# Optimization experiments

Hardware: AMD Instinct MI355X
Metric: run time of the kernel (lower is better)

Reference implementation:

```python
import jax, jax.numpy as jnp
import numpy as np

B, N = 2, 2048
N_FEAT, N_HID, N_HEADS, N_CLASS = 256, 64, 8, 16
ALPHA = 0.2  # leakyrelu negative slope
NEG_INF = -1.0e12


def _xavier_uniform(key, shape, gain=1.414):
    fan_in, fan_out = shape[-2], shape[-1]
    bound = gain * np.sqrt(6.0 / (fan_in + fan_out))
    return jax.random.uniform(key, shape, jnp.float32, -bound, bound)


def setup_inputs() -> dict:
    key = jax.random.key(0)
    k_x, k_adj, k_w, k_a, k_wo, k_ao = jax.random.split(key, 6)
    x = jax.random.normal(k_x, (B, N, N_FEAT), jnp.float32)
    adj = (jax.random.uniform(k_adj, (B, N, N)) < 0.005).astype(jnp.float32)
    adj = jnp.maximum(adj, jnp.eye(N, dtype=jnp.float32))  # self loops
    Ws = _xavier_uniform(k_w, (N_HEADS, N_FEAT, N_HID))
    As = _xavier_uniform(k_a, (N_HEADS, 2 * N_HID, 1))
    W_out = _xavier_uniform(k_wo, (N_HID * N_HEADS, N_CLASS))
    a_out = _xavier_uniform(k_ao, (2 * N_CLASS, 1))
    return {"x": x, "adj": adj, "Ws": Ws, "As": As,
            "W_out": W_out, "a_out": a_out, "d_window": 3}


def init_weight_graph(adj, d_window):
    # Faithful vectorized version of GAT.init_weight_graph (the per-batch
    # python loop is just a vmap over batch; adj_graphs list is dead code).
    Nn = adj.shape[-1]
    eye = jnp.eye(Nn, dtype=adj.dtype)
    sigma2 = 2.0 * (d_window / 2.0) ** 2
    # NOTE: original uses np.exp(-1 ** 2 / sigma2) == exp(-1/sigma2) (python precedence)
    weight = eye + np.float32(np.exp(-1.0 / sigma2)) * (adj - eye)
    prev = adj
    for i in range(d_window - 1):
        e_prev = jnp.einsum('bij,bkj->bik', prev, adj)          # prev @ adj^T
        e_ret = (e_prev > 0).astype(adj.dtype)
        e_graph = ((e_ret - prev) > 0).astype(adj.dtype)
        weight = weight + np.float32(np.exp(-(i + 2) ** 2 / sigma2)) * e_graph
        prev = e_ret
    return weight  # [B, N, N]


def gat_layer(x, W, a, adjw, concat):
    h = jnp.einsum('bnf,fo->bno', x, W)                         # [B,N,F_out]
    F_out = W.shape[1]
    # cat([h_i, h_j]) @ a  ==  (h@a1)_i + (h@a2)_j  (exact same math, no N^2*2F tensor)
    f1 = jnp.einsum('bno,o->bn', h, a[:F_out, 0])
    f2 = jnp.einsum('bno,o->bn', h, a[F_out:, 0])
    e = jax.nn.leaky_relu(f1[:, :, None] + f2[:, None, :], ALPHA)  # [B,N,N]
    attention = jnp.where(adjw > 0, adjw * e, NEG_INF)
    attention = jax.nn.softmax(attention, axis=2)
    # dropout is a no-op in eval mode
    h_prime = jnp.einsum('bnm,bmo->bno', attention, h)
    return jax.nn.elu(h_prime) if concat else h_prime


def reference(x, adj, Ws, As, W_out, a_out, d_window):
    adjw = init_weight_graph(adj, d_window)
    # multi-head layers (concat=True), vmapped over heads then concatenated
    heads = jax.vmap(lambda W, a: gat_layer(x, W, a, adjw, True))(Ws, As)  # [H,B,N,nhid]
    Hh, Bb, Nn, Fh = heads.shape
    xh = jnp.moveaxis(heads, 0, 2).reshape(Bb, Nn, Hh * Fh)
    out = gat_layer(xh, W_out, a_out, adjw, False)
    return jax.nn.elu(out)  # [B, N, n_class]
```

## Files before the change

kernel.cpp:

```cpp
#include <hip/hip_runtime.h>
#include <stdint.h>

#define NB 2
#define NN 2048
#define NF 256
#define NHID 64
#define NH 8
#define NC 16
#define NW 64
#define LRA 0.2f

constexpr double L2E_D = 1.4426950408889634;
constexpr float L2E  = (float)L2E_D;
constexpr float K12  = (float)((0.8007374029168081 - 0.4111122905071874) * L2E_D);
constexpr float K23  = (float)((0.4111122905071874 - 0.1353352832366127) * L2E_D);
constexpr float K3L  = (float)(0.1353352832366127 * L2E_D);
constexpr float KD   = K12 + (K23 + K3L);
constexpr float GB   = 1e30f;

using short8  = __attribute__((ext_vector_type(8))) short;
using floatx4 = __attribute__((ext_vector_type(4))) float;
union Frag { short8 v; uint32_t w[4]; };

__device__ __forceinline__ float bf2f(uint16_t h){ return __uint_as_float(((uint32_t)h) << 16); }
__device__ __forceinline__ uint16_t f2bf(float f){
  uint32_t u = __float_as_uint(f);
  return (uint16_t)((u + 0x7FFFu + ((u >> 16) & 1u)) >> 16);
}
__device__ __forceinline__ float lrelu(float x){ return fmaxf(x, LRA * x); }
__device__ __forceinline__ void pack2(float p0, float p1, uint32_t& hi, uint32_t& lo){
  uint32_t u0 = __float_as_uint(p0), u1 = __float_as_uint(p1);
  hi = __builtin_amdgcn_perm(u1, u0, 0x07060302u);
  float t0 = p0 - __uint_as_float(u0 & 0xFFFF0000u);
  float t1 = p1 - __uint_as_float(u1 & 0xFFFF0000u);
  lo = __builtin_amdgcn_perm(__float_as_uint(t1), __float_as_uint(t0), 0x07060302u);
}
__device__ __forceinline__ uint32_t packrn2(float p0, float p1){
  uint32_t u0 = __float_as_uint(p0), u1 = __float_as_uint(p1);
  u0 += 0x7FFFu + ((u0 >> 16) & 1u);
  u1 += 0x7FFFu + ((u1 >> 16) & 1u);
  return __builtin_amdgcn_perm(u1, u0, 0x07060302u);
}

__global__ void __launch_bounds__(256) k_pack(const uint32_t* __restrict__ adj,
                                              const float* __restrict__ Ws,
                                              uint32_t* __restrict__ adjR,
                                              uint32_t* __restrict__ colB,
                                              uint16_t* __restrict__ WTh,
                                              uint16_t* __restrict__ WTl){
  __shared__ uint32_t tile[64][65];
  int jc = blockIdx.x, kc = blockIdx.y, b = blockIdx.z;
  int t = threadIdx.x, lane = t & 63, w = t >> 6;
  int k0 = kc * 64, j0 = jc * 64;
  const uint32_t* base = adj + ((size_t)b * NN + k0) * NN + j0;
  for (int s = 0; s < 16; ++s){
    int r = w * 16 + s;
    tile[r][lane] = base[(size_t)r * NN + lane] << 1;
  }
  __syncthreads();
  for (int s = 0; s < 16; ++s){
    int r = s * 4 + w;
    uint64_t mr = __ballot(tile[r][lane] != 0u);
    if (lane < 2) adjR[((size_t)b * NN + k0 + r) * NW + jc * 2 + lane] = (uint32_t)(mr >> (32 * lane));
    uint64_t mc = __ballot(tile[lane][r] != 0u);
    if (lane < 2) colB[((size_t)b * NN + j0 + r) * NW + kc * 2 + lane] = (uint32_t)(mc >> (32 * lane));
  }
  if (kc == 0 && b == 0 && jc < NH){
    int hd = jc;
    const float* src = Ws + (size_t)hd * NF * NHID;
    for (int s = 0; s < 64; ++s){
      int f = s * 4 + (t >> 6), o = t & 63;
      float v = src[(size_t)f * NHID + o];
      uint16_t hi = f2bf(v);
      uint16_t lo = f2bf(v - bf2f(hi));
      WTh[(size_t)hd * NHID * NF + (size_t)o * NF + f] = hi;
      WTl[(size_t)hd * NHID * NF + (size_t)o * NF + f] = lo;
    }
  }
}

__global__ void __launch_bounds__(256, 4) k_rh(const uint32_t* __restrict__ adjR,
                                               const uint32_t* __restrict__ colB,
                                               uint32_t* __restrict__ cmb,
                                               const float* __restrict__ x,
                                               const uint16_t* __restrict__ WTh,
                                               const uint16_t* __restrict__ WTl,
                                               const float* __restrict__ As,
                                               uint16_t* __restrict__ hTh,
                                               float* __restrict__ f1,
                                               float* __restrict__ f2){
  __shared__ float hbuf[16][65];
  int t = threadIdx.x, lane = t & 63, w = t >> 6;
  if (blockIdx.x < 1024){
    int row = blockIdx.x * 4 + w;
    int b = row >> 11;
    const uint32_t* colb = colB + (size_t)b * NN * NW + lane;
    uint32_t myadj = adjR[(size_t)row * NW + lane];
    uint32_t acc2 = 0;
    for (int ww = 0; ww < 64; ++ww){
      uint32_t bits = __shfl(myadj, ww);
      const uint32_t* cb = colb + (size_t)(ww * 32) * NW;
      while (bits){
        int b0 = __ffs(bits) - 1;              bits &= bits - 1;
        int b1 = bits ? __ffs(bits) - 1 : b0;  bits &= bits - 1;
        int b2 = bits ? __ffs(bits) - 1 : b0;  bits &= bits - 1;
        int b3 = bits ? __ffs(bits) - 1 : b0;  bits &= bits - 1;
        uint32_t v0 = cb[(size_t)b0 * NW];
        uint32_t v1 = cb[(size_t)b1 * NW];
        uint32_t v2 = cb[(size_t)b2 * NW];
        uint32_t v3 = cb[(size_t)b3 * NW];
        acc2 |= (v0 | v1) | (v2 | v3);
      }
    }
    uint32_t acc3 = 0;
    for (int ww = 0; ww < 64; ++ww){
      uint32_t bits = __shfl(acc2, ww);
      const uint32_t* cb = colb + (size_t)(ww * 32) * NW;
      while (bits){
        int b0 = __ffs(bits) - 1;              bits &= bits - 1;
        int b1 = bits ? __ffs(bits) - 1 : b0;  bits &= bits - 1;
        int b2 = bits ? __ffs(bits) - 1 : b0;  bits &= bits - 1;
        int b3 = bits ? __ffs(bits) - 1 : b0;  bits &= bits - 1;
        uint32_t v0 = cb[(size_t)b0 * NW];
        uint32_t v1 = cb[(size_t)b1 * NW];
        uint32_t v2 = cb[(size_t)b2 * NW];
        uint32_t v3 = cb[(size_t)b3 * NW];
        acc3 |= (v0 | v1) | (v2 | v3);
      }
    }
    uint32_t* cw = cmb + ((size_t)row * NW + lane) * 3;
    cw[0] = myadj; cw[1] = acc2; cw[2] = acc3;
  } else {
    int bid2 = blockIdx.x - 1024;
    int itile = bid2 & 127, hd = (bid2 >> 7) & 7, b = bid2 >> 10;
    int q = lane >> 4, m = lane & 15;
    int n0 = itile * 16;
    floatx4 acc = {0.f, 0.f, 0.f, 0.f};
    const float*    xrow = x   + ((size_t)b * NN + n0 + m) * NF;
    const uint16_t* wth  = WTh + ((size_t)hd * NHID + w * 16 + m) * NF;
    const uint16_t* wtl  = WTl + ((size_t)hd * NHID + w * 16 + m) * NF;
    for (int k0 = 0; k0 < NF; k0 += 32){
      float4 xa = *(const float4*)(xrow + k0 + q * 8);
      float4 xb = *(const float4*)(xrow + k0 + q * 8 + 4);
      float xv[8] = {xa.x, xa.y, xa.z, xa.w, xb.x, xb.y, xb.z, xb.w};
      Frag ah, al;
      #pragma unroll
      for (int k = 0; k < 4; ++k) pack2(xv[2*k], xv[2*k+1], ah.w[k], al.w[k]);
      short8 bh = *(const short8*)(wth + k0 + q * 8);
      short8 bl = *(const short8*)(wtl + k0 + q * 8);
      acc = __builtin_amdgcn_mfma_f32_16x16x32_bf16(ah.v, bh, acc, 0, 0, 0);
      acc = __builtin_amdgcn_mfma_f32_16x16x32_bf16(al.v, bh, acc, 0, 0, 0);
      acc = __builtin_amdgcn_mfma_f32_16x16x32_bf16(ah.v, bl, acc, 0, 0, 0);
    }
    #pragma unroll
    for (int v = 0; v < 4; ++v) hbuf[q * 4 + v][w * 16 + m] = acc[v];
    __syncthreads();
    {
      int o = t >> 2, nb = (t & 3) * 4;
      uint64_t pkh = 0;
      for (int s = 0; s < 4; ++s)
        pkh |= (uint64_t)f2bf(hbuf[nb + s][o]) << (16 * s);
      size_t off = ((size_t)(b * NH + hd) * NHID + o) * NN + n0 + nb;
      *(uint64_t*)(hTh + off) = pkh;
    }
    float a1v = As[hd * 128 + lane];
    float a2v = As[hd * 128 + 64 + lane];
    for (int s = 0; s < 4; ++s){
      int row = w * 4 + s;
      float hv = hbuf[row][lane];
      float v1 = hv * a1v, v2 = hv * a2v;
      for (int d = 1; d < 64; d <<= 1){ v1 += __shfl_xor(v1, d); v2 += __shfl_xor(v2, d); }
      if (lane == 0){
        f1[(size_t)(b * NH + hd) * NN + n0 + row] = v1;
        f2[(size_t)(b * NH + hd) * NN + n0 + row] = v2;
      }
    }
  }
}

__global__ void __launch_bounds__(512) k_attn1(const uint32_t* __restrict__ cmb,
                                               const float* __restrict__ f1,
                                               const float* __restrict__ f2,
                                               const uint16_t* __restrict__ hTh,
                                               float* __restrict__ xh){
  int combo = blockIdx.x * 2 + blockIdx.y;
  int hd = combo & 7, b = combo >> 3;
  int itile = blockIdx.z;
  int t = threadIdx.x, lane = t & 63, w = t >> 6;
  int q = lane >> 4, m = lane & 15;
  int i0 = itile * 32;
  int igA = i0 + m, igB = i0 + 16 + m;
  const float* f1p = f1 + (size_t)(b * NH + hd) * NN;
  const float* f2p = f2 + (size_t)(b * NH + hd) * NN;
  float f1A = f1p[igA], f1B = f1p[igB];
  const uint32_t* cA = cmb + ((size_t)b * NN + igA) * (NW * 3);
  const uint32_t* cB = cmb + ((size_t)b * NN + igB) * (NW * 3);
  size_t hoff = (size_t)(b * NH + hd) * NHID * NN;
  const uint16_t* hhp = hTh + hoff;
  int jlo = w * 256, sh = q * 8;
  floatx4 aA0 = {0.f,0.f,0.f,0.f}, aA1 = aA0, aA2 = aA0, aA3 = aA0;
  floatx4 aB0 = aA0, aB1 = aA0, aB2 = aA0, aB3 = aA0;
  float lsA = 0.f, lsB = 0.f;
  for (int s = 0; s < 8; ++s){
    int j0 = jlo + s * 32;
    int wi = j0 >> 5;
    const uint32_t* cwA = cA + wi * 3;
    const uint32_t* cwB = cB + wi * 3;
    uint32_t waA = cwA[0] >> sh, w2A = cwA[1] >> sh, w3A = cwA[2] >> sh;
    uint32_t waB = cwB[0] >> sh, w2B = cwB[1] >> sh, w3B = cwB[2] >> sh;
    const float4 fa = *(const float4*)(f2p + j0 + sh);
    const float4 fb = *(const float4*)(f2p + j0 + sh + 4);
    float f2v[8] = {fa.x, fa.y, fa.z, fa.w, fb.x, fb.y, fb.z, fb.w};
    float pvA[8], pvB[8];
    #pragma unroll
    for (int u = 0; u < 8; ++u){
      float eA = lrelu(f1A + f2v[u]);
      float b1 = (float)((waA >> u) & 1u);
      float b2 = (float)((w2A >> u) & 1u);
      float b3 = (float)((w3A >> u) & 1u);
      float Ks = fmaf(b1, K12, fmaf(b2, K23, K3L));
      float p = exp2f(fmaf(eA, Ks, fmaf(b3, GB, -GB)));
      pvA[u] = p; lsA += p;
      float eB = lrelu(f1B + f2v[u]);
      float c1 = (float)((waB >> u) & 1u);
      float c2 = (float)((w2B >> u) & 1u);
      float c3 = (float)((w3B >> u) & 1u);
      float Kt = fmaf(c1, K12, fmaf(c2, K23, K3L));
      float pb = exp2f(fmaf(eB, Kt, fmaf(c3, GB, -GB)));
      pvB[u] = pb; lsB += pb;
    }
    Frag ahA, ahB;
    #pragma unroll
    for (int k = 0; k < 4; ++k){
      ahA.w[k] = packrn2(pvA[2*k], pvA[2*k+1]);
      ahB.w[k] = packrn2(pvB[2*k], pvB[2*k+1]);
    }
    const uint16_t* hrow_h = hhp + j0 + sh;
    #pragma unroll
    for (int blk = 0; blk < 4; ++blk){
      size_t ro = (size_t)(blk * 16 + m) * NN;
      short8 bh = *(const short8*)(hrow_h + ro);
      floatx4* apA = (blk == 0) ? &aA0 : (blk == 1) ? &aA1 : (blk == 2) ? &aA2 : &aA3;
      floatx4* apB = (blk == 0) ? &aB0 : (blk == 1) ? &aB1 : (blk == 2) ? &aB2 : &aB3;
      *apA = __builtin_amdgcn_mfma_f32_16x16x32_bf16(ahA.v, bh, *apA, 0, 0, 0);
      *apB = __builtin_amdgcn_mfma_f32_16x16x32_bf16(ahB.v, bh, *apB, 0, 0, 0);
    }
  }
  lsA += __shfl_xor(lsA, 16); lsA += __shfl_xor(lsA, 32);
  lsB += __shfl_xor(lsB, 16); lsB += __shfl_xor(lsB, 32);
  __shared__ float redO[4][32][66];
  __shared__ float redl[8][32];
  if (lane < 16) redl[w][lane] = lsA;
  else if (lane < 32) redl[w][16 + (lane & 15)] = lsB;
  if (w < 4){
    #pragma unroll
    for (int v = 0; v < 4; ++v){
      int r = q * 4 + v;
      redO[w][r][ 0 + m] = aA0[v];
      redO[w][r][16 + m] = aA1[v];
      redO[w][r][32 + m] = aA2[v];
      redO[w][r][48 + m] = aA3[v];
      redO[w][16 + r][ 0 + m] = aB0[v];
      redO[w][16 + r][16 + m] = aB1[v];
      redO[w][16 + r][32 + m] = aB2[v];
      redO[w][16 + r][48 + m] = aB3[v];
    }
  }
  __syncthreads();
  if (w >= 4){
    int wb = w - 4;
    #pragma unroll
    for (int v = 0; v < 4; ++v){
      int r = q * 4 + v;
      redO[wb][r][ 0 + m] += aA0[v];
      redO[wb][r][16 + m] += aA1[v];
      redO[wb][r][32 + m] += aA2[v];
      redO[wb][r][48 + m] += aA3[v];
      redO[wb][16 + r][ 0 + m] += aB0[v];
      redO[wb][16 + r][16 + m] += aB1[v];
      redO[wb][16 + r][32 + m] += aB2[v];
      redO[wb][16 + r][48 + m] += aB3[v];
    }
  }
  __syncthreads();
  int col = t & 63, r0 = t >> 6;
  const float* f1row = f1p + i0;
  #pragma unroll
  for (int s2 = 0; s2 < 4; ++s2){
    int row = s2 * 8 + r0;
    int i = i0 + row;
    float ov = (redO[0][row][col] + redO[1][row][col]) + (redO[2][row][col] + redO[3][row][col]);
    float lv = ((redl[0][row] + redl[1][row]) + (redl[2][row] + redl[3][row]))
             + ((redl[4][row] + redl[5][row]) + (redl[6][row] + redl[7][row]));
    float eii = lrelu(f1row[row] + f2p[i]);
    float pcorr = exp2f(eii * L2E) - exp2f(eii * KD);
    float hic = bf2f(hhp[(size_t)col * NN + i]);
    ov += pcorr * hic;
    lv += pcorr;
    lv = fmaxf(lv, 1e-30f);
    float vv = ov / lv;
    vv = vv > 0.f ? vv : expm1f(vv);
    xh[(size_t)(b * NN + i) * (NH * NHID) + hd * NHID + col] = vv;
  }
}

__global__ void __launch_bounds__(256) k_outprep(const float* __restrict__ xh,
                                                 const float* __restrict__ W_out,
                                                 const float* __restrict__ a_out,
                                                 uint16_t* __restrict__ h2Th,
                                                 float* __restrict__ f12,
                                                 float* __restrict__ f22){
  int t = threadIdx.x, lane = t & 63, w = t >> 6;
  int row = blockIdx.x * 4 + w;
  int b = row >> 11, n = row & (NN - 1);
  int o = lane & 15, c = lane >> 4;
  const float* xr = xh + (size_t)row * (NH * NHID) + c * 128;
  const float* wp = W_out + (size_t)(c * 128) * NC + o;
  float a0 = 0.f, a1 = 0.f, a2 = 0.f, a3 = 0.f;
  #pragma unroll 4
  for (int f = 0; f < 128; f += 4){
    float4 xv = *(const float4*)(xr + f);
    a0 = fmaf(xv.x, wp[(size_t)(f + 0) * NC], a0);
    a1 = fmaf(xv.y, wp[(size_t)(f + 1) * NC], a1);
    a2 = fmaf(xv.z, wp[(size_t)(f + 2) * NC], a2);
    a3 = fmaf(xv.w, wp[(size_t)(f + 3) * NC], a3);
  }
  float acc = (a0 + a1) + (a2 + a3);
  acc += __shfl_xor(acc, 16); acc += __shfl_xor(acc, 32);
  if (lane < 16) h2Th[((size_t)b * NC + o) * NN + n] = f2bf(acc);
  float v1 = acc * a_out[o];
  float v2 = acc * a_out[NC + o];
  for (int d = 1; d < 16; d <<= 1){ v1 += __shfl_xor(v1, d); v2 += __shfl_xor(v2, d); }
  if (lane == 0){ f12[row] = v1; f22[row] = v2; }
}

__global__ void __launch_bounds__(512) k_attn2(const uint32_t* __restrict__ cmb,
                                               const float* __restrict__ f12,
                                               const float* __restrict__ f22,
                                               const uint16_t* __restrict__ h2Th,
                                               float* __restrict__ out){
  int itile = blockIdx.x, b = blockIdx.z;
  int t = threadIdx.x, lane = t & 63, w = t >> 6;
  int q = lane >> 4, m = lane & 15;
  int i0 = itile * 16, ig = i0 + m;
  float f1v = f12[(size_t)b * NN + ig];
  const float*    f2p = f22 + (size_t)b * NN;
  const uint32_t* cA = cmb + ((size_t)b * NN + ig) * (NW * 3);
  const uint16_t* hhp = h2Th + (size_t)b * NC * NN;
  int jlo = w * 256, sh = q * 8;
  floatx4 ac = {0.f,0.f,0.f,0.f};
  float ls0 = 0.f, ls1 = 0.f;
  for (int s = 0; s < 8; ++s){
    int j0 = jlo + s * 32;
    int wi = j0 >> 5;
    const uint32_t* cw = cA + wi * 3;
    uint32_t wa = cw[0] >> sh, w2 = cw[1] >> sh, w3 = cw[2] >> sh;
    const float4 fa = *(const float4*)(f2p + j0 + sh);
    const float4 fb = *(const float4*)(f2p + j0 + sh + 4);
    float f2v[8] = {fa.x, fa.y, fa.z, fa.w, fb.x, fb.y, fb.z, fb.w};
    float pv[8];
    #pragma unroll
    for (int u = 0; u < 8; ++u){
      float e = lrelu(f1v + f2v[u]);
      float b1 = (float)((wa >> u) & 1u);
      float b2 = (float)((w2 >> u) & 1u);
      float b3 = (float)((w3 >> u) & 1u);
      float Ks = fmaf(b1, K12, fmaf(b2, K23, K3L));
      float p = exp2f(fmaf(e, Ks, fmaf(b3, GB, -GB)));
      pv[u] = p;
      if (u & 1) ls1 += p; else ls0 += p;
    }
    Frag afh;
    #pragma unroll
    for (int k = 0; k < 4; ++k) afh.w[k] = packrn2(pv[2*k], pv[2*k+1]);
    size_t ro = (size_t)m * NN + j0 + sh;
    short8 bh = *(const short8*)(hhp + ro);
    ac = __builtin_amdgcn_mfma_f32_16x16x32_bf16(afh.v, bh, ac, 0, 0, 0);
  }
  float lsum = ls0 + ls1;
  lsum += __shfl_xor(lsum, 16); lsum += __shfl_xor(lsum, 32);
  __shared__ float redO[4][16][17];
  __shared__ float redl[8][16];
  if (lane < 16) redl[w][lane] = lsum;
  if (w < 4){
    #pragma unroll
    for (int v = 0; v < 4; ++v) redO[w][q * 4 + v][m] = ac[v];
  }
  __syncthreads();
  if (w >= 4){
    int wb = w - 4;
    #pragma unroll
    for (int v = 0; v < 4; ++v) redO[wb][q * 4 + v][m] += ac[v];
  }
  __syncthreads();
  if (t < 256){
    int col = t & 15, row = t >> 4;
    int i = i0 + row;
    float ov = (redO[0][row][col] + redO[1][row][col]) + (redO[2][row][col] + redO[3][row][col]);
    float lv = ((redl[0][row] + redl[1][row]) + (redl[2][row] + redl[3][row]))
             + ((redl[4][row] + redl[5][row]) + (redl[6][row] + redl[7][row]));
    float eii = lrelu(f12[(size_t)b * NN + i] + f2p[i]);
    float pcorr = exp2f(eii * L2E) - exp2f(eii * KD);
    float hic = bf2f(hhp[(size_t)col * NN + i]);
    ov += pcorr * hic;
    lv += pcorr;
    lv = fmaxf(lv, 1e-30f);
    float vv = ov / lv;
    vv = vv > 0.f ? vv : expm1f(vv);
    out[(size_t)(b * NN + i) * NC + col] = vv;
  }
}

extern "C" void kernel_launch(void* const* d_in, const int* in_sizes, int n_in,
                              void* d_out, int out_size, void* d_ws, size_t ws_size,
                              hipStream_t stream) {
  const float* x        = (const float*)d_in[0];
  const uint32_t* adj_u = (const uint32_t*)d_in[1];
  const float* Ws    = (const float*)d_in[2];
  const float* As    = (const float*)d_in[3];
  const float* W_out = (const float*)d_in[4];
  const float* a_out = (const float*)d_in[5];
  float* out = (float*)d_out;

  char* ws = (char*)d_ws;
  const size_t MB = 1u << 20;
  uint32_t* adjR = (uint32_t*)(ws + 0 * MB);
  uint32_t* colB = (uint32_t*)(ws + 1 * MB);
  uint32_t* cmb  = (uint32_t*)(ws + 2 * MB);
  uint16_t* WTh  = (uint16_t*)(ws + 5 * MB);
  uint16_t* WTl  = (uint16_t*)(ws + 5 * MB + 256 * 1024);
  float*    f1   = (float*)(ws + 5 * MB + 512 * 1024);
  float*    f2   = (float*)(ws + 5 * MB + 640 * 1024);
  uint16_t* hTh  = (uint16_t*)(ws + 6 * MB);
  float*    xh   = (float*)(ws + 14 * MB);
  uint16_t* h2Th = (uint16_t*)(ws + 22 * MB);
  float*    f12  = (float*)(ws + 22 * MB + 256 * 1024);
  float*    f22  = (float*)(ws + 22 * MB + 272 * 1024);

  k_pack   <<<dim3(32, 32, NB), 256, 0, stream>>>(adj_u, Ws, adjR, colB, WTh, WTl);
  k_rh     <<<dim3(1024 + NN / 16 * NH * NB), 256, 0, stream>>>(adjR, colB, cmb,
                                             x, WTh, WTl, As, hTh, f1, f2);
  k_attn1  <<<dim3(8, 2, NN / 32), 512, 0, stream>>>(cmb, f1, f2, hTh, xh);
  k_outprep<<<dim3(1024), 256, 0, stream>>>(xh, W_out, a_out, h2Th, f12, f22);
  k_attn2  <<<dim3(NN / 16, 1, NB), 512, 0, stream>>>(cmb, f12, f22, h2Th, out);
}
```

Measured before the change: 243.4 us.

## Tile attention kernel over two heads per row tile instead of 32 rows

```diff
diff --git a/kernel.cpp b/kernel.cpp
--- a/kernel.cpp
+++ b/kernel.cpp
@@ -183,20 +183,21 @@
                                                const float* __restrict__ f2,
                                                const uint16_t* __restrict__ hTh,
                                                float* __restrict__ xh){
-  int combo = blockIdx.x * 2 + blockIdx.y;
-  int hd = combo & 7, b = combo >> 3;
+  int combo = blockIdx.x;
+  int hp = combo & 3, b = combo >> 2;
+  int h0 = hp * 2, h1 = h0 + 1;
   int itile = blockIdx.z;
   int t = threadIdx.x, lane = t & 63, w = t >> 6;
   int q = lane >> 4, m = lane & 15;
-  int i0 = itile * 32;
-  int igA = i0 + m, igB = i0 + 16 + m;
-  const float* f1p = f1 + (size_t)(b * NH + hd) * NN;
-  const float* f2p = f2 + (size_t)(b * NH + hd) * NN;
-  float f1A = f1p[igA], f1B = f1p[igB];
-  const uint32_t* cA = cmb + ((size_t)b * NN + igA) * (NW * 3);
-  const uint32_t* cB = cmb + ((size_t)b * NN + igB) * (NW * 3);
-  size_t hoff = (size_t)(b * NH + hd) * NHID * NN;
-  const uint16_t* hhp = hTh + hoff;
+  int i0 = itile * 16, ig = i0 + m;
+  const float* f1p0 = f1 + (size_t)(b * NH + h0) * NN;
+  const float* f2p0 = f2 + (size_t)(b * NH + h0) * NN;
+  const float* f1p1 = f1 + (size_t)(b * NH + h1) * NN;
+  const float* f2p1 = f2 + (size_t)(b * NH + h1) * NN;
+  float f1A0 = f1p0[ig], f1A1 = f1p1[ig];
+  const uint32_t* cA = cmb + ((size_t)b * NN + ig) * (NW * 3);
+  const uint16_t* hhp0 = hTh + (size_t)(b * NH + h0) * NHID * NN;
+  const uint16_t* hhp1 = hTh + (size_t)(b * NH + h1) * NHID * NN;
   int jlo = w * 256, sh = q * 8;
   floatx4 aA0 = {0.f,0.f,0.f,0.f}, aA1 = aA0, aA2 = aA0, aA3 = aA0;
   floatx4 aB0 = aA0, aB1 = aA0, aB2 = aA0, aB3 = aA0;
@@ -204,46 +205,46 @@
   for (int s = 0; s < 8; ++s){
     int j0 = jlo + s * 32;
     int wi = j0 >> 5;
-    const uint32_t* cwA = cA + wi * 3;
-    const uint32_t* cwB = cB + wi * 3;
-    uint32_t waA = cwA[0] >> sh, w2A = cwA[1] >> sh, w3A = cwA[2] >> sh;
-    uint32_t waB = cwB[0] >> sh, w2B = cwB[1] >> sh, w3B = cwB[2] >> sh;
-    const float4 fa = *(const float4*)(f2p + j0 + sh);
-    const float4 fb = *(const float4*)(f2p + j0 + sh + 4);
-    float f2v[8] = {fa.x, fa.y, fa.z, fa.w, fb.x, fb.y, fb.z, fb.w};
-    float pvA[8], pvB[8];
+    const uint32_t* cw = cA + wi * 3;
+    uint32_t wa = cw[0] >> sh, w2 = cw[1] >> sh, w3 = cw[2] >> sh;
+    const float4 fa0 = *(const float4*)(f2p0 + j0 + sh);
+    const float4 fb0 = *(const float4*)(f2p0 + j0 + sh + 4);
+    const float4 fa1 = *(const float4*)(f2p1 + j0 + sh);
+    const float4 fb1 = *(const float4*)(f2p1 + j0 + sh + 4);
+    float f2v0[8] = {fa0.x, fa0.y, fa0.z, fa0.w, fb0.x, fb0.y, fb0.z, fb0.w};
+    float f2v1[8] = {fa1.x, fa1.y, fa1.z, fa1.w, fb1.x, fb1.y, fb1.z, fb1.w};
+    float pv0[8], pv1[8];
     #pragma unroll
     for (int u = 0; u < 8; ++u){
-      float eA = lrelu(f1A + f2v[u]);
-      float b1 = (float)((waA >> u) & 1u);
-      float b2 = (float)((w2A >> u) & 1u);
-      float b3 = (float)((w3A >> u) & 1u);
+      float b1 = (float)((wa >> u) & 1u);
+      float b2 = (float)((w2 >> u) & 1u);
+      float b3 = (float)((w3 >> u) & 1u);
       float Ks = fmaf(b1, K12, fmaf(b2, K23, K3L));
-      float p = exp2f(fmaf(eA, Ks, fmaf(b3, GB, -GB)));
-      pvA[u] = p; lsA += p;
-      float eB = lrelu(f1B + f2v[u]);
-      float c1 = (float)((waB >> u) & 1u);
-      float c2 = (float)((w2B >> u) & 1u);
-      float c3 = (float)((w3B >> u) & 1u);
-      float Kt = fmaf(c1, K12, fmaf(c2, K23, K3L));
-      float pb = exp2f(fmaf(eB, Kt, fmaf(c3, GB, -GB)));
-      pvB[u] = pb; lsB += pb;
-    }
-    Frag ahA, ahB;
+      float bias = fmaf(b3, GB, -GB);
+      float e0 = lrelu(f1A0 + f2v0[u]);
+      float p0 = exp2f(fmaf(e0, Ks, bias));
+      pv0[u] = p0; lsA += p0;
+      float e1 = lrelu(f1A1 + f2v1[u]);
+      float p1 = exp2f(fmaf(e1, Ks, bias));
+      pv1[u] = p1; lsB += p1;
+    }
+    Frag ah0, ah1;
     #pragma unroll
     for (int k = 0; k < 4; ++k){
-      ahA.w[k] = packrn2(pvA[2*k], pvA[2*k+1]);
-      ahB.w[k] = packrn2(pvB[2*k], pvB[2*k+1]);
-    }
-    const uint16_t* hrow_h = hhp + j0 + sh;
+      ah0.w[k] = packrn2(pv0[2*k], pv0[2*k+1]);
+      ah1.w[k] = packrn2(pv1[2*k], pv1[2*k+1]);
+    }
+    const uint16_t* hr0 = hhp0 + j0 + sh;
+    const uint16_t* hr1 = hhp1 + j0 + sh;
     #pragma unroll
     for (int blk = 0; blk < 4; ++blk){
       size_t ro = (size_t)(blk * 16 + m) * NN;
-      short8 bh = *(const short8*)(hrow_h + ro);
+      short8 bh0 = *(const short8*)(hr0 + ro);
+      short8 bh1 = *(const short8*)(hr1 + ro);
       floatx4* apA = (blk == 0) ? &aA0 : (blk == 1) ? &aA1 : (blk == 2) ? &aA2 : &aA3;
       floatx4* apB = (blk == 0) ? &aB0 : (blk == 1) ? &aB1 : (blk == 2) ? &aB2 : &aB3;
-      *apA = __builtin_amdgcn_mfma_f32_16x16x32_bf16(ahA.v, bh, *apA, 0, 0, 0);
-      *apB = __builtin_amdgcn_mfma_f32_16x16x32_bf16(ahB.v, bh, *apB, 0, 0, 0);
+      *apA = __builtin_amdgcn_mfma_f32_16x16x32_bf16(ah0.v, bh0, *apA, 0, 0, 0);
+      *apB = __builtin_amdgcn_mfma_f32_16x16x32_bf16(ah1.v, bh1, *apB, 0, 0, 0);
     }
   }
   lsA += __shfl_xor(lsA, 16); lsA += __shfl_xor(lsA, 32);
@@ -284,23 +285,27 @@
   }
   __syncthreads();
   int col = t & 63, r0 = t >> 6;
-  const float* f1row = f1p + i0;
   #pragma unroll
   for (int s2 = 0; s2 < 4; ++s2){
     int row = s2 * 8 + r0;
-    int i = i0 + row;
+    int hsel = row >> 4;
+    int i = i0 + (row & 15);
+    const float* f1e = hsel ? f1p1 : f1p0;
+    const float* f2e = hsel ? f2p1 : f2p0;
+    const uint16_t* hh = hsel ? hhp1 : hhp0;
+    int hdv = hsel ? h1 : h0;
     float ov = (redO[0][row][col] + redO[1][row][col]) + (redO[2][row][col] + redO[3][row][col]);
     float lv = ((redl[0][row] + redl[1][row]) + (redl[2][row] + redl[3][row]))
              + ((redl[4][row] + redl[5][row]) + (redl[6][row] + redl[7][row]));
-    float eii = lrelu(f1row[row] + f2p[i]);
+    float eii = lrelu(f1e[i] + f2e[i]);
     float pcorr = exp2f(eii * L2E) - exp2f(eii * KD);
-    float hic = bf2f(hhp[(size_t)col * NN + i]);
+    float hic = bf2f(hh[(size_t)col * NN + i]);
     ov += pcorr * hic;
     lv += pcorr;
     lv = fmaxf(lv, 1e-30f);
     float vv = ov / lv;
     vv = vv > 0.f ? vv : expm1f(vv);
-    xh[(size_t)(b * NN + i) * (NH * NHID) + hd * NHID + col] = vv;
+    xh[(size_t)(b * NN + i) * (NH * NHID) + hdv * NHID + col] = vv;
   }
 }
 
@@ -440,7 +445,7 @@
   k_pack   <<<dim3(32, 32, NB), 256, 0, stream>>>(adj_u, Ws, adjR, colB, WTh, WTl);
   k_rh     <<<dim3(1024 + NN / 16 * NH * NB), 256, 0, stream>>>(adjR, colB, cmb,
                                              x, WTh, WTl, As, hTh, f1, f2);
-  k_attn1  <<<dim3(8, 2, NN / 32), 512, 0, stream>>>(cmb, f1, f2, hTh, xh);
+  k_attn1  <<<dim3(8, 1, NN / 16), 512, 0, stream>>>(cmb, f1, f2, hTh, xh);
   k_outprep<<<dim3(1024), 256, 0, stream>>>(xh, W_out, a_out, h2Th, f12, f22);
   k_attn2  <<<dim3(NN / 16, 1, NB), 512, 0, stream>>>(cmb, f12, f22, h2Th, out);
 }
```

Result: slower. 265.4 us (+9.0%).

## Compact two-hop neighbor list in LDS and widen attn2 blocks to 16 waves

Applied to the files above, without the earlier changes.

```diff
diff --git a/kernel.cpp b/kernel.cpp
--- a/kernel.cpp
+++ b/kernel.cpp
@@ -9,6 +9,7 @@
 #define NC 16
 #define NW 64
 #define LRA 0.2f
+#define RCAP 1024
 
 constexpr double L2E_D = 1.4426950408889634;
 constexpr float L2E  = (float)L2E_D;
@@ -90,10 +91,11 @@
                                                float* __restrict__ f1,
                                                float* __restrict__ f2){
   __shared__ float hbuf[16][65];
+  __shared__ uint16_t lst[4][RCAP];
   int t = threadIdx.x, lane = t & 63, w = t >> 6;
   if (blockIdx.x < 1024){
     int row = blockIdx.x * 4 + w;
-    int b = row >> 11;
+    int b = row >> 11, iloc = row & (NN - 1);
     const uint32_t* colb = colB + (size_t)b * NN * NW + lane;
     uint32_t myadj = adjR[(size_t)row * NW + lane];
     uint32_t acc2 = 0;
@@ -112,21 +114,43 @@
         acc2 |= (v0 | v1) | (v2 | v3);
       }
     }
+    int cnt = __popc(acc2);
+    int inc = cnt;
+    #pragma unroll
+    for (int d = 1; d < 64; d <<= 1){
+      int v = __shfl_up(inc, d);
+      if (lane >= d) inc += v;
+    }
+    int total = __shfl(inc, 63);
+    int n = inc - cnt;
+    uint32_t bits = acc2;
+    while (bits){
+      int bt = __ffs(bits) - 1; bits &= bits - 1;
+      if (n < RCAP) lst[w][n] = (uint16_t)((lane << 5) + bt);
+      ++n;
+    }
+    total = min(total, RCAP);
+    int pad = (8 - (total & 7)) & 7;
+    if (lane < pad && total + lane < RCAP) lst[w][total + lane] = (uint16_t)iloc;
+    int total8 = min(total + pad, RCAP);
+    __syncthreads();
     uint32_t acc3 = 0;
-    for (int ww = 0; ww < 64; ++ww){
-      uint32_t bits = __shfl(acc2, ww);
-      const uint32_t* cb = colb + (size_t)(ww * 32) * NW;
-      while (bits){
-        int b0 = __ffs(bits) - 1;              bits &= bits - 1;
-        int b1 = bits ? __ffs(bits) - 1 : b0;  bits &= bits - 1;
-        int b2 = bits ? __ffs(bits) - 1 : b0;  bits &= bits - 1;
-        int b3 = bits ? __ffs(bits) - 1 : b0;  bits &= bits - 1;
-        uint32_t v0 = cb[(size_t)b0 * NW];
-        uint32_t v1 = cb[(size_t)b1 * NW];
-        uint32_t v2 = cb[(size_t)b2 * NW];
-        uint32_t v3 = cb[(size_t)b3 * NW];
-        acc3 |= (v0 | v1) | (v2 | v3);
-      }
+    const uint32_t* cb0 = colB + (size_t)b * NN * NW + lane;
+    for (int k = 0; k < total8; k += 8){
+      uint4 qw = *(const uint4*)&lst[w][k];
+      uint32_t i0 = qw.x & 0xFFFFu, i1 = qw.x >> 16;
+      uint32_t i2 = qw.y & 0xFFFFu, i3 = qw.y >> 16;
+      uint32_t i4 = qw.z & 0xFFFFu, i5 = qw.z >> 16;
+      uint32_t i6 = qw.w & 0xFFFFu, i7 = qw.w >> 16;
+      uint32_t v0 = cb0[(size_t)i0 * NW];
+      uint32_t v1 = cb0[(size_t)i1 * NW];
+      uint32_t v2 = cb0[(size_t)i2 * NW];
+      uint32_t v3 = cb0[(size_t)i3 * NW];
+      uint32_t v4 = cb0[(size_t)i4 * NW];
+      uint32_t v5 = cb0[(size_t)i5 * NW];
+      uint32_t v6 = cb0[(size_t)i6 * NW];
+      uint32_t v7 = cb0[(size_t)i7 * NW];
+      acc3 |= ((v0 | v1) | (v2 | v3)) | ((v4 | v5) | (v6 | v7));
     }
     uint32_t* cw = cmb + ((size_t)row * NW + lane) * 3;
     cw[0] = myadj; cw[1] = acc2; cw[2] = acc3;
@@ -334,11 +358,11 @@
   if (lane == 0){ f12[row] = v1; f22[row] = v2; }
 }
 
-__global__ void __launch_bounds__(512) k_attn2(const uint32_t* __restrict__ cmb,
-                                               const float* __restrict__ f12,
-                                               const float* __restrict__ f22,
-                                               const uint16_t* __restrict__ h2Th,
-                                               float* __restrict__ out){
+__global__ void __launch_bounds__(1024) k_attn2(const uint32_t* __restrict__ cmb,
+                                                const float* __restrict__ f12,
+                                                const float* __restrict__ f22,
+                                                const uint16_t* __restrict__ h2Th,
+                                                float* __restrict__ out){
   int itile = blockIdx.x, b = blockIdx.z;
   int t = threadIdx.x, lane = t & 63, w = t >> 6;
   int q = lane >> 4, m = lane & 15;
@@ -347,10 +371,10 @@
   const float*    f2p = f22 + (size_t)b * NN;
   const uint32_t* cA = cmb + ((size_t)b * NN + ig) * (NW * 3);
   const uint16_t* hhp = h2Th + (size_t)b * NC * NN;
-  int jlo = w * 256, sh = q * 8;
+  int jlo = w * 128, sh = q * 8;
   floatx4 ac = {0.f,0.f,0.f,0.f};
   float ls0 = 0.f, ls1 = 0.f;
-  for (int s = 0; s < 8; ++s){
+  for (int s = 0; s < 4; ++s){
     int j0 = jlo + s * 32;
     int wi = j0 >> 5;
     const uint32_t* cw = cA + wi * 3;
@@ -379,16 +403,16 @@
   }
   float lsum = ls0 + ls1;
   lsum += __shfl_xor(lsum, 16); lsum += __shfl_xor(lsum, 32);
-  __shared__ float redO[4][16][17];
-  __shared__ float redl[8][16];
+  __shared__ float redO[8][16][17];
+  __shared__ float redl[16][16];
   if (lane < 16) redl[w][lane] = lsum;
-  if (w < 4){
+  if (w < 8){
     #pragma unroll
     for (int v = 0; v < 4; ++v) redO[w][q * 4 + v][m] = ac[v];
   }
   __syncthreads();
-  if (w >= 4){
-    int wb = w - 4;
+  if (w >= 8){
+    int wb = w - 8;
     #pragma unroll
     for (int v = 0; v < 4; ++v) redO[wb][q * 4 + v][m] += ac[v];
   }
@@ -396,9 +420,11 @@
   if (t < 256){
     int col = t & 15, row = t >> 4;
     int i = i0 + row;
-    float ov = (redO[0][row][col] + redO[1][row][col]) + (redO[2][row][col] + redO[3][row][col]);
-    float lv = ((redl[0][row] + redl[1][row]) + (redl[2][row] + redl[3][row]))
-             + ((redl[4][row] + redl[5][row]) + (redl[6][row] + redl[7][row]));
+    float ov = ((redO[0][row][col] + redO[1][row][col]) + (redO[2][row][col] + redO[3][row][col]))
+             + ((redO[4][row][col] + redO[5][row][col]) + (redO[6][row][col] + redO[7][row][col]));
+    float lv = 0.f;
+    #pragma unroll
+    for (int k = 0; k < 16; ++k) lv += redl[k][row];
     float eii = lrelu(f12[(size_t)b * NN + i] + f2p[i]);
     float pcorr = exp2f(eii * L2E) - exp2f(eii * KD);
     float hic = bf2f(hhp[(size_t)col * NN + i]);
@@ -442,5 +468,5 @@
                                              x, WTh, WTl, As, hTh, f1, f2);
   k_attn1  <<<dim3(8, 2, NN / 32), 512, 0, stream>>>(cmb, f1, f2, hTh, xh);
   k_outprep<<<dim3(1024), 256, 0, stream>>>(xh, W_out, a_out, h2Th, f12, f22);
-  k_attn2  <<<dim3(NN / 16, 1, NB), 512, 0, stream>>>(cmb, f12, f22, h2Th, out);
-}
+  k_attn2  <<<dim3(NN / 16, 1, NB), 1024, 0, stream>>>(cmb, f12, f22, h2Th, out);
+}
```

Measured after the change: 226.0 us. 7.1% less time.
